# Kernel optimization log

Hardware: AMD Instinct MI355X
Metric: run time of the kernel (lower is better)

Reference implementation:

```python
import jax, jax.numpy as jnp
import numpy as np

NVFP4_VALUES = jnp.array([0.0, 0.5, 1.0, 1.5, 2.0, 3.0, 4.0, 6.0], dtype=jnp.float32)
NVFP4_MAX = 6.0


def quantize_to_nvfp4(t):
    """Fake-quantize to NVFP4 (e2m1) via nearest codebook magnitude.
    Returns (quantized_tensor, inv_scale) matching the torch reference."""
    amax = jnp.maximum(jnp.max(jnp.abs(t)), 1e-12)
    scale = NVFP4_MAX / amax                      # scalar
    scaled = jnp.clip(t.astype(jnp.float32) * scale, -NVFP4_MAX, NVFP4_MAX)
    signs = jnp.sign(scaled)
    # distance to each of the 8 e2m1 magnitudes -> nearest index
    dist = jnp.abs(jnp.abs(scaled)[..., None] - NVFP4_VALUES)  # (..., 8)
    idx = jnp.argmin(dist, axis=-1)
    quantized = signs * NVFP4_VALUES[idx]
    return quantized, 1.0 / scale


def setup_inputs() -> dict:
    key = jax.random.key(0)
    kx, kw = jax.random.split(key)
    x = jax.random.normal(kx, (512, 4096), dtype=jnp.float32)          # batch=512 (in SUPPORTED_BATCH_SIZES -> no padding)
    # kaiming-uniform-ish init for weight [out_features, in_features]
    bound = float(np.sqrt(6.0 / 4096.0))
    weight = jax.random.uniform(kw, (4096, 4096), dtype=jnp.float32,
                                minval=-bound, maxval=bound)
    return {"x": x, "weight": weight}


def reference(x, weight):
    # batch==512 is an exact supported size, so pad/unpad is identity.
    x_q, x_inv_scale = quantize_to_nvfp4(x)
    w_q, w_inv_scale = quantize_to_nvfp4(weight)
    # out[b,o] = sum_i (x_q*x_s)[b,i] * (w_q*w_s)[o,i]
    out = jnp.einsum('bi,oi->bo', x_q * x_inv_scale, w_q * w_inv_scale)
    return out.astype(x.dtype)
```

## Files before the change

### kernel.cpp

```cpp
#include <hip/hip_runtime.h>

#define M_DIM 512
#define N_DIM 4096
#define K_DIM 4096

typedef __attribute__((ext_vector_type(4))) float f32x4;

#define PART_X_OFF 0
#define PART_X_N   256
#define PART_W_OFF 256
#define PART_W_N   1024
#define AMAX_OFF   1280
#define XQ_BYTE_OFF 8192
#define WQ_BYTE_OFF (XQ_BYTE_OFF + M_DIM * K_DIM)

__global__ __launch_bounds__(256) void amax_kernel(
    const float4* __restrict__ x4, const float4* __restrict__ w4,
    float* __restrict__ ws_f) {
    const int b = blockIdx.x;
    float m = 0.0f;
    if (b < PART_X_N) {
        const int n4 = M_DIM * K_DIM / 4, stride = PART_X_N * 256;
        for (int i = b * 256 + threadIdx.x; i < n4; i += stride) {
            float4 a = x4[i];
            m = fmaxf(m, fmaxf(fmaxf(fabsf(a.x), fabsf(a.y)),
                               fmaxf(fabsf(a.z), fabsf(a.w))));
        }
    } else {
        const int n4 = N_DIM * K_DIM / 4, stride = PART_W_N * 256;
        for (int i = (b - PART_X_N) * 256 + threadIdx.x; i < n4; i += stride) {
            float4 a = w4[i];
            m = fmaxf(m, fmaxf(fmaxf(fabsf(a.x), fabsf(a.y)),
                               fmaxf(fabsf(a.z), fabsf(a.w))));
        }
    }
    for (int off = 32; off > 0; off >>= 1)
        m = fmaxf(m, __shfl_down(m, off, 64));
    __shared__ float sm[4];
    if ((threadIdx.x & 63) == 0) sm[threadIdx.x >> 6] = m;
    __syncthreads();
    if (threadIdx.x == 0) {
        m = fmaxf(fmaxf(sm[0], sm[1]), fmaxf(sm[2], sm[3]));
        ws_f[(b < PART_X_N) ? (PART_X_OFF + b) : (PART_W_OFF + b - PART_X_N)] = m;
    }
}

__device__ __forceinline__ unsigned int q1(float x, float s) {
    float a = fabsf(x) * s;
    unsigned int b;
    if      (a <= 0.25f) b = 0x00u;
    else if (a <= 0.75f) b = 0x30u;
    else if (a <= 1.25f) b = 0x38u;
    else if (a <= 1.75f) b = 0x3Cu;
    else if (a <= 2.5f)  b = 0x40u;
    else if (a <= 3.5f)  b = 0x44u;
    else if (a <= 5.0f)  b = 0x48u;
    else                 b = 0x4Cu;
    return b | ((__float_as_uint(x) >> 24) & 0x80u);
}
__device__ __forceinline__ unsigned int qpack4(float4 v, float s) {
    return q1(v.x, s) | (q1(v.y, s) << 8) | (q1(v.z, s) << 16) | (q1(v.w, s) << 24);
}

__global__ __launch_bounds__(256) void quant_kernel(
    const float4* __restrict__ x4, const float4* __restrict__ w4,
    float* __restrict__ ws_f, unsigned char* __restrict__ ws_b) {
    const int b = blockIdx.x, t = threadIdx.x;
    const bool is_x = b < 512;
    float m = 0.0f;
    if (is_x) {
        m = ws_f[PART_X_OFF + t];
    } else {
        for (int i = t; i < PART_W_N; i += 256)
            m = fmaxf(m, ws_f[PART_W_OFF + i]);
    }
    for (int off = 32; off > 0; off >>= 1)
        m = fmaxf(m, __shfl_down(m, off, 64));
    __shared__ float sm[4];
    if ((t & 63) == 0) sm[t >> 6] = m;
    __syncthreads();
    m = fmaxf(fmaxf(sm[0], sm[1]), fmaxf(sm[2], sm[3]));
    float amax = fmaxf(m, 1e-12f);
    float s = 6.0f / amax;
    if (t == 0 && b == 0)   ws_f[AMAX_OFF + 0] = amax;
    if (t == 0 && b == 512) ws_f[AMAX_OFF + 1] = amax;

    const float4* src = is_x ? x4 : w4;
    unsigned char* dstb = ws_b + (is_x ? XQ_BYTE_OFF : WQ_BYTE_OFF);
    const int idx16 = (is_x ? b : b - 512) * 256 + t;
    const float4* p = src + (size_t)idx16 * 4;
    uint4 o;
    o.x = qpack4(p[0], s);
    o.y = qpack4(p[1], s);
    o.z = qpack4(p[2], s);
    o.w = qpack4(p[3], s);
    ((uint4*)dstb)[idx16] = o;
}

__device__ __forceinline__ void async_copy16(const void* g, void* l) {
    __builtin_amdgcn_global_load_lds(
        (const __attribute__((address_space(1))) unsigned int*)g,
        (__attribute__((address_space(3))) unsigned int*)l, 16, 0, 0);
}

__global__ __launch_bounds__(256, 2) void gemm_kernel(
    const unsigned char* __restrict__ A, const unsigned char* __restrict__ B,
    float* __restrict__ C, const float* __restrict__ amax2) {
    __shared__ __align__(16) unsigned char As[64 * 512];
    __shared__ __align__(16) unsigned char Bs[64 * 512];

    const int bid  = blockIdx.x;
    const int bm   = (bid >> 6) * 64;
    const int bn   = ((bid & 7) * 8 + ((bid >> 3) & 7)) * 64;
    const int tid  = threadIdx.x;
    const int lane = tid & 63;
    const int wave = tid >> 6;
    const int wm   = (wave >> 1) * 32;
    const int wn   = (wave & 1) * 32;
    const int t15  = lane & 15;
    const int quad = lane >> 4;

    const float cs = (1.0f / (6.0f / fmaxf(amax2[0], 1e-12f))) *
                     (1.0f / (6.0f / fmaxf(amax2[1], 1e-12f)));

    const unsigned char* agp[8];
    const unsigned char* bgp[8];
#pragma unroll
    for (int j = 0; j < 8; j++) {
        const int c = j * 256 + tid;
        const int row = c >> 5, pcol = c & 31;
        const int gk = pcol ^ (row & 31);
        agp[j] = A + (size_t)(bm + row) * K_DIM + gk * 16;
        bgp[j] = B + (size_t)(bn + row) * K_DIM + gk * 16;
    }

    f32x4 acc[2][2] = {};
    const int ra0 = wm + t15, ra1 = ra0 + 16;
    const int rb0 = wn + t15, rb1 = rb0 + 16;
    const int qh = quad >> 1, qb = (quad & 1) * 8;

    for (int ko = 0; ko < K_DIM; ko += 512) {
#pragma unroll
        for (int j = 0; j < 8; j++) {
            async_copy16(agp[j] + ko, As + (j * 256 + tid) * 16);
            async_copy16(bgp[j] + ko, Bs + (j * 256 + tid) * 16);
        }
        __syncthreads();

#pragma unroll
        for (int kb = 0; kb < 16; kb++) {
            const int g = 2 * kb + qh;
            const long a0 = *(const long*)(As + ra0 * 512 + ((g ^ (ra0 & 31)) * 16) + qb);
            const long a1 = *(const long*)(As + ra1 * 512 + ((g ^ (ra1 & 31)) * 16) + qb);
            const long b0 = *(const long*)(Bs + rb0 * 512 + ((g ^ (rb0 & 31)) * 16) + qb);
            const long b1 = *(const long*)(Bs + rb1 * 512 + ((g ^ (rb1 & 31)) * 16) + qb);
            acc[0][0] = __builtin_amdgcn_mfma_f32_16x16x32_fp8_fp8(a0, b0, acc[0][0], 0, 0, 0);
            acc[0][1] = __builtin_amdgcn_mfma_f32_16x16x32_fp8_fp8(a0, b1, acc[0][1], 0, 0, 0);
            acc[1][0] = __builtin_amdgcn_mfma_f32_16x16x32_fp8_fp8(a1, b0, acc[1][0], 0, 0, 0);
            acc[1][1] = __builtin_amdgcn_mfma_f32_16x16x32_fp8_fp8(a1, b1, acc[1][1], 0, 0, 0);
        }
        __syncthreads();
    }

#pragma unroll
    for (int i = 0; i < 2; i++)
#pragma unroll
        for (int j = 0; j < 2; j++) {
            const int m0 = bm + wm + i * 16 + quad * 4;
            const int n0 = bn + wn + j * 16 + t15;
#pragma unroll
            for (int r = 0; r < 4; r++)
                C[(size_t)(m0 + r) * N_DIM + n0] = acc[i][j][r] * cs;
        }
}

extern "C" void kernel_launch(void* const* d_in, const int* in_sizes, int n_in,
                              void* d_out, int out_size, void* d_ws, size_t ws_size,
                              hipStream_t stream) {
    const float* x = (const float*)d_in[0];
    const float* w = (const float*)d_in[1];
    float* out = (float*)d_out;

    float* ws_f = (float*)d_ws;
    unsigned char* ws_b = (unsigned char*)d_ws;
    const unsigned char* xq = ws_b + XQ_BYTE_OFF;
    const unsigned char* wq = ws_b + WQ_BYTE_OFF;

    amax_kernel<<<PART_X_N + PART_W_N, 256, 0, stream>>>(
        (const float4*)x, (const float4*)w, ws_f);
    quant_kernel<<<512 + 4096, 256, 0, stream>>>(
        (const float4*)x, (const float4*)w, ws_f, ws_b);
    gemm_kernel<<<(M_DIM / 64) * (N_DIM / 64), 256, 0, stream>>>(
        xq, wq, out, ws_f + AMAX_OFF);
}
```

Before: 135.8 us.

## Switch GEMM to 32x32x16 FP8 MFMA with intra-block split-K across waves

Replaces the 2x2 grid of 16x16x32 FP8 MFMAs per wave with 32x32x16 MFMAs. Each pair of waves covers a 32-row slab, and the two wave pairs split the K dimension of each LDS tile. Partial sums from the second half are reduced through shared memory before the scaled store. The intent is fewer LDS reads per MFMA and better operand reuse from the larger instruction. The cost is an extra LDS reduction and sync at the end, and 32 accumulator registers per fragment.

```diff
diff --git a/kernel.cpp b/kernel.cpp
--- a/kernel.cpp
+++ b/kernel.cpp
@@ -4,7 +4,7 @@
 #define N_DIM 4096
 #define K_DIM 4096
 
-typedef __attribute__((ext_vector_type(4))) float f32x4;
+typedef __attribute__((ext_vector_type(16))) float f32x16;
 
 #define PART_X_OFF 0
 #define PART_X_N   256
@@ -115,10 +115,10 @@
     const int tid  = threadIdx.x;
     const int lane = tid & 63;
     const int wave = tid >> 6;
-    const int wm   = (wave >> 1) * 32;
-    const int wn   = (wave & 1) * 32;
-    const int t15  = lane & 15;
-    const int quad = lane >> 4;
+    const int pr   = wave & 1;
+    const int kh   = wave >> 1;
+    const int l31  = lane & 31;
+    const int koff = (lane >> 5) * 8;
 
     const float cs = (1.0f / (6.0f / fmaxf(amax2[0], 1e-12f))) *
                      (1.0f / (6.0f / fmaxf(amax2[1], 1e-12f)));
@@ -134,10 +134,10 @@
         bgp[j] = B + (size_t)(bn + row) * K_DIM + gk * 16;
     }
 
-    f32x4 acc[2][2] = {};
-    const int ra0 = wm + t15, ra1 = ra0 + 16;
-    const int rb0 = wn + t15, rb1 = rb0 + 16;
-    const int qh = quad >> 1, qb = (quad & 1) * 8;
+    f32x16 acc[2] = {};
+    const unsigned char* arow = As + (pr * 32 + l31) * 512;
+    const unsigned char* brow0 = Bs + l31 * 512;
+    const unsigned char* brow1 = Bs + (32 + l31) * 512;
 
     for (int ko = 0; ko < K_DIM; ko += 512) {
 #pragma unroll
@@ -148,30 +148,40 @@
         __syncthreads();
 
 #pragma unroll
-        for (int kb = 0; kb < 16; kb++) {
-            const int g = 2 * kb + qh;
-            const long a0 = *(const long*)(As + ra0 * 512 + ((g ^ (ra0 & 31)) * 16) + qb);
-            const long a1 = *(const long*)(As + ra1 * 512 + ((g ^ (ra1 & 31)) * 16) + qb);
-            const long b0 = *(const long*)(Bs + rb0 * 512 + ((g ^ (rb0 & 31)) * 16) + qb);
-            const long b1 = *(const long*)(Bs + rb1 * 512 + ((g ^ (rb1 & 31)) * 16) + qb);
-            acc[0][0] = __builtin_amdgcn_mfma_f32_16x16x32_fp8_fp8(a0, b0, acc[0][0], 0, 0, 0);
-            acc[0][1] = __builtin_amdgcn_mfma_f32_16x16x32_fp8_fp8(a0, b1, acc[0][1], 0, 0, 0);
-            acc[1][0] = __builtin_amdgcn_mfma_f32_16x16x32_fp8_fp8(a1, b0, acc[1][0], 0, 0, 0);
-            acc[1][1] = __builtin_amdgcn_mfma_f32_16x16x32_fp8_fp8(a1, b1, acc[1][1], 0, 0, 0);
+        for (int s = 0; s < 16; s++) {
+            const int g = kh * 16 + s;
+            const int off = ((g ^ l31) * 16) + koff;
+            const long a0 = *(const long*)(arow + off);
+            const long b0 = *(const long*)(brow0 + off);
+            const long b1 = *(const long*)(brow1 + off);
+            acc[0] = __builtin_amdgcn_mfma_f32_32x32x16_fp8_fp8(a0, b0, acc[0], 0, 0, 0);
+            acc[1] = __builtin_amdgcn_mfma_f32_32x32x16_fp8_fp8(a0, b1, acc[1], 0, 0, 0);
         }
         __syncthreads();
     }
 
-#pragma unroll
-    for (int i = 0; i < 2; i++)
-#pragma unroll
-        for (int j = 0; j < 2; j++) {
-            const int m0 = bm + wm + i * 16 + quad * 4;
-            const int n0 = bn + wn + j * 16 + t15;
-#pragma unroll
-            for (int r = 0; r < 4; r++)
-                C[(size_t)(m0 + r) * N_DIM + n0] = acc[i][j][r] * cs;
-        }
+    float* scratch = (float*)As;
+    if (kh == 1) {
+#pragma unroll
+        for (int j = 0; j < 2; j++)
+#pragma unroll
+            for (int r = 0; r < 16; r++) {
+                const int rl = (r & 3) + 8 * (r >> 2) + 4 * (lane >> 5);
+                scratch[pr * 2048 + rl * 64 + j * 32 + l31] = acc[j][r];
+            }
+    }
+    __syncthreads();
+    if (kh == 0) {
+#pragma unroll
+        for (int j = 0; j < 2; j++)
+#pragma unroll
+            for (int r = 0; r < 16; r++) {
+                const int rl = (r & 3) + 8 * (r >> 2) + 4 * (lane >> 5);
+                const float v = (acc[j][r] +
+                                 scratch[pr * 2048 + rl * 64 + j * 32 + l31]) * cs;
+                C[(size_t)(bm + pr * 32 + rl) * N_DIM + bn + j * 32 + l31] = v;
+            }
+    }
 }
 
 extern "C" void kernel_launch(void* const* d_in, const int* in_sizes, int n_in,
```

Result: slower. 139.7 us (+2.8%).
